# Kernel optimization log

Measured on AMD Instinct MI355X. Metric: run time of the kernel, lower is better.

## Reference

```python
import jax, jax.numpy as jnp
import numpy as np

N = 100000
E = 1600000
F_IN = 128
HID = 128
C = 10
NEG_SLOPE = 0.2


def setup_inputs() -> dict:
    key = jax.random.key(0)
    ks = jax.random.split(key, 12)
    x = jax.random.normal(ks[0], (N, F_IN), dtype=jnp.float32)
    edge_index = jax.random.randint(ks[1], (2, E), 0, N, dtype=jnp.int64)
    batch = jnp.zeros((N,), dtype=jnp.int64)
    s1 = 1.0 / np.sqrt(F_IN)
    s2 = 1.0 / np.sqrt(HID)
    return {
        "x": x,
        "edge_index": edge_index,
        "batch": batch,
        "W1": jax.random.normal(ks[2], (F_IN, HID), dtype=jnp.float32) * s1,
        "a_src1": jax.random.normal(ks[3], (HID,), dtype=jnp.float32) * s2,
        "a_dst1": jax.random.normal(ks[4], (HID,), dtype=jnp.float32) * s2,
        "b1": jnp.zeros((HID,), dtype=jnp.float32),
        "W2": jax.random.normal(ks[5], (HID, HID), dtype=jnp.float32) * s2,
        "a_src2": jax.random.normal(ks[6], (HID,), dtype=jnp.float32) * s2,
        "a_dst2": jax.random.normal(ks[7], (HID,), dtype=jnp.float32) * s2,
        "b2": jnp.zeros((HID,), dtype=jnp.float32),
        "Wlin": jax.random.normal(ks[8], (HID, C), dtype=jnp.float32) * s2,
        "blin": jnp.zeros((C,), dtype=jnp.float32),
    }


def gat_conv(x, src, dst, W, a_src, a_dst, b):
    # PyG GATConv, heads=1: h = xW; alpha_e = softmax_dst(leaky_relu(a_src.h[src] + a_dst.h[dst]))
    h = x @ W                                  # [N, H]
    alpha_s = h @ a_src                        # [N]
    alpha_d = h @ a_dst                        # [N]
    e = jax.nn.leaky_relu(alpha_s[src] + alpha_d[dst], NEG_SLOPE)  # [E]
    m = jax.ops.segment_max(e, dst, num_segments=N)                # per-dst max (stable softmax)
    ex = jnp.exp(e - m[dst])
    denom = jax.ops.segment_sum(ex, dst, num_segments=N)
    alpha = ex / (denom[dst] + 1e-16)          # [E]
    out = jax.ops.segment_sum(h[src] * alpha[:, None], dst, num_segments=N)
    return out + b


def reference(x, edge_index, batch, W1, a_src1, a_dst1, b1, W2, a_src2, a_dst2, b2, Wlin, blin):
    x = x.astype(jnp.float32)
    loops = jnp.arange(N, dtype=edge_index.dtype)
    src = jnp.concatenate([edge_index[0], loops])  # add_self_loops=True
    dst = jnp.concatenate([edge_index[1], loops])
    h = jax.nn.relu(gat_conv(x, src, dst, W1, a_src1, a_dst1, b1))
    h = jax.nn.relu(gat_conv(h, src, dst, W2, a_src2, a_dst2, b2))
    # dropout(p=0.5) is identity in eval mode
    return h @ Wlin + blin
```

## Files before the change

### kernel.cpp

```cpp
#include <hip/hip_runtime.h>

#define N_NODES 100000
#define N_EDGES 1600000
#define TOTE    (N_EDGES + N_NODES)
#define NEG     0.2f
#define NB      ((N_NODES + 255) >> 8)
#define BCAP    5120

typedef __attribute__((ext_vector_type(8))) short bf16x8;
typedef __attribute__((ext_vector_type(4))) float floatx4;

__device__ __forceinline__ unsigned short f2bf(float f) {
  unsigned int u = __float_as_uint(f);
  u += 0x7fffu + ((u >> 16) & 1u);
  return (unsigned short)(u >> 16);
}
__device__ __forceinline__ float bf_lo(unsigned int r) { return __uint_as_float(r << 16); }
__device__ __forceinline__ float bf_hi(unsigned int r) { return __uint_as_float(r & 0xffff0000u); }

__global__ __launch_bounds__(256) void k_wprep(const float* __restrict__ W1, const float* __restrict__ W2,
                                               unsigned short* __restrict__ B1hi, unsigned short* __restrict__ B1lo,
                                               unsigned short* __restrict__ B2hi, unsigned short* __restrict__ B2lo,
                                               int* __restrict__ bucketCnt) {
  int b = blockIdx.x;
  int t = threadIdx.x;
  if (b == 16) {
    for (int i = t; i < NB * 16; i += 256) bucketCnt[i] = 0;
    return;
  }
  const float* W = (b < 8) ? W1 : W2;
  unsigned short* Bh = (b < 8) ? B1hi : B2hi;
  unsigned short* Bl = (b < 8) ? B1lo : B2lo;
  int ntile = b & 7;
  int kq = t >> 6, lane = t & 63;
  int q = lane >> 4, m = lane & 15;
  int n = ntile * 16 + m;
  union { unsigned short us[8]; uint4 u4; } hi, lo;
#pragma unroll
  for (int j = 0; j < 8; ++j) {
    int k = kq * 32 + q * 8 + j;
    float w = W[(size_t)k * 128 + n];
    unsigned int u = __float_as_uint(w);
    hi.us[j] = (unsigned short)(u >> 16);
    float res = w - __uint_as_float(u & 0xffff0000u);
    lo.us[j] = f2bf(res);
  }
  size_t fo = ((size_t)(ntile * 4 + kq) * 64 + lane) * 8;
  *reinterpret_cast<uint4*>(Bh + fo) = hi.u4;
  *reinterpret_cast<uint4*>(Bl + fo) = lo.u4;
}

__global__ __launch_bounds__(256) void k_binA(const int* __restrict__ ei, int* __restrict__ bucketCnt,
                                              unsigned int* __restrict__ binned) {
  __shared__ int hist[NB];
  __shared__ int cur[NB];
  int t = threadIdx.x;
  for (int b = t; b < NB; b += 256) hist[b] = 0;
  __syncthreads();
  unsigned int pk[16]; int bk[16];
#pragma unroll
  for (int j = 0; j < 16; ++j) {
    int idx = blockIdx.x * 4096 + j * 256 + t;
    if (idx < N_EDGES) {
      int s = ei[idx], d = ei[N_EDGES + idx];
      bk[j] = d >> 8;
      pk[j] = ((unsigned int)s << 8) | (unsigned int)(d & 255);
      atomicAdd(&hist[bk[j]], 1);
    } else bk[j] = -1;
  }
  __syncthreads();
  for (int b = t; b < NB; b += 256) {
    int h = hist[b];
    if (h) cur[b] = b * BCAP + atomicAdd(&bucketCnt[b * 16], h);
  }
  __syncthreads();
#pragma unroll
  for (int j = 0; j < 16; ++j) {
    if (bk[j] >= 0) {
      int pos = atomicAdd(&cur[bk[j]], 1);
      binned[pos] = pk[j];
    }
  }
}

__global__ __launch_bounds__(512) void k_bin_scan(const int* __restrict__ bucketCnt,
                                                  int* __restrict__ binOffs) {
  __shared__ int sc[512];
  int t = threadIdx.x;
  int v = (t < NB) ? bucketCnt[t * 16] : 0;
  sc[t] = v; __syncthreads();
  for (int off = 1; off < 512; off <<= 1) {
    int x = (t >= off) ? sc[t - off] : 0;
    __syncthreads();
    sc[t] += x;
    __syncthreads();
  }
  int excl = sc[t] - v;
  if (t <= NB) binOffs[t] = excl;
}

__global__ __launch_bounds__(256) void k_binB(const unsigned int* __restrict__ binned,
                                              const int* __restrict__ binOffs,
                                              int* __restrict__ offs, int* __restrict__ srcs) {
  __shared__ int cnt[256];
  __shared__ int sc[256];
  __shared__ int cur[256];
  int b = blockIdx.x;
  int t = threadIdx.x;
  int node0 = b << 8;
  int nNodes = min(256, N_NODES - node0);
  int cntE = binOffs[b + 1] - binOffs[b];
  int e0 = b * BCAP, e1 = e0 + cntE;
  int base = binOffs[b] + node0;

  cnt[t] = 0; __syncthreads();
  for (int i = e0 + t; i < e1; i += 256) atomicAdd(&cnt[binned[i] & 255u], 1);
  __syncthreads();

  int v = (t < nNodes) ? cnt[t] + 1 : 0;
  sc[t] = v; __syncthreads();
  for (int off = 1; off < 256; off <<= 1) {
    int x = (t >= off) ? sc[t - off] : 0;
    __syncthreads();
    sc[t] += x;
    __syncthreads();
  }
  int excl = sc[t] - v;
  if (t < nNodes) {
    offs[node0 + t] = base + excl;
    srcs[base + excl] = node0 + t;
  }
  cur[t] = excl + 1;
  __syncthreads();

  for (int i = e0 + t; i < e1; i += 256) {
    unsigned int e = binned[i];
    int j = (int)(e & 255u);
    int s = (int)(e >> 8);
    int p = atomicAdd(&cur[j], 1);
    srcs[base + p] = s;
  }
  if (b == 0 && t == 0) offs[N_NODES] = TOTE;
}

template <bool SPLIT>
__global__ __launch_bounds__(256, 4) void k_gemm_mfma(const void* __restrict__ Aptr,
                                                   const unsigned short* __restrict__ Bhi,
                                                   const unsigned short* __restrict__ Blo,
                                                   unsigned short* __restrict__ Cb,
                                                   const float* __restrict__ avS, const float* __restrict__ avD,
                                                   float* __restrict__ aS, float* __restrict__ aD,
                                                   float* __restrict__ slotS, float* __restrict__ slotD) {
  constexpr int SRCB  = SPLIT ? 512 : 256;
  constexpr int ROWB  = SPLIT ? 528 : 272;
  constexpr int ABYTES = 64 * ROWB;
  constexpr int CHUNKS = ABYTES / 1024;
  __shared__ char sbuf[ABYTES];
  __shared__ float redS[64 * 4], redD[64 * 4];
  __shared__ float mS[64], mD[64];
  int t = threadIdx.x;
  int w = t >> 6, lane = t & 63;
  int q = lane >> 4, m = lane & 15;
  int rbase = blockIdx.x * 64;
  const char* Ab = (const char*)Aptr;

  for (int c = w; c < CHUNKS; c += 4) {
    int L = c * 1024 + lane * 16;
    int r = L / ROWB;
    int off = L - r * ROWB;
    int gr = min(rbase + r, N_NODES - 1);
    const char* src = (off < SRCB) ? (Ab + (size_t)gr * SRCB + off) : Ab;
    __builtin_amdgcn_global_load_lds((const __attribute__((address_space(1))) void*)src,
                                     (__attribute__((address_space(3))) void*)(sbuf + c * 1024),
                                     16, 0, 0);
  }

  floatx4 acc[4][2];
#pragma unroll
  for (int mt = 0; mt < 4; ++mt)
#pragma unroll
    for (int nt = 0; nt < 2; ++nt) acc[mt][nt] = (floatx4){0.f, 0.f, 0.f, 0.f};

  __syncthreads();

#pragma unroll
  for (int k0 = 0; k0 < 4; ++k0) {
    bf16x8 Bh[2], Bl[2], Ah[4], Al[4];
#pragma unroll
    for (int nt = 0; nt < 2; ++nt) {
      int ntg = w * 2 + nt;
      size_t fo = ((size_t)(ntg * 4 + k0) * 64 + lane) * 8;
      Bh[nt] = *reinterpret_cast<const bf16x8*>(Bhi + fo);
      Bl[nt] = *reinterpret_cast<const bf16x8*>(Blo + fo);
    }
#pragma unroll
    for (int mt = 0; mt < 4; ++mt) {
      int R = mt * 16 + m;
      if constexpr (SPLIT) {
        const char* ap = sbuf + R * ROWB + k0 * 128 + q * 32;
        float4 v0 = *reinterpret_cast<const float4*>(ap);
        float4 v1 = *reinterpret_cast<const float4*>(ap + 16);
        float av[8] = {v0.x, v0.y, v0.z, v0.w, v1.x, v1.y, v1.z, v1.w};
        union { unsigned short us[8]; bf16x8 v; } uh, ul;
#pragma unroll
        for (int j = 0; j < 8; ++j) {
          unsigned int u = __float_as_uint(av[j]);
          uh.us[j] = (unsigned short)(u >> 16);
          float res = av[j] - __uint_as_float(u & 0xffff0000u);
          ul.us[j] = f2bf(res);
        }
        Ah[mt] = uh.v; Al[mt] = ul.v;
      } else {
        Ah[mt] = *reinterpret_cast<const bf16x8*>(sbuf + R * ROWB + k0 * 64 + q * 16);
      }
    }
#pragma unroll
    for (int mt = 0; mt < 4; ++mt)
#pragma unroll
      for (int nt = 0; nt < 2; ++nt) {
        acc[mt][nt] = __builtin_amdgcn_mfma_f32_16x16x32_bf16(Ah[mt], Bh[nt], acc[mt][nt], 0, 0, 0);
        acc[mt][nt] = __builtin_amdgcn_mfma_f32_16x16x32_bf16(Ah[mt], Bl[nt], acc[mt][nt], 0, 0, 0);
        if constexpr (SPLIT)
          acc[mt][nt] = __builtin_amdgcn_mfma_f32_16x16x32_bf16(Al[mt], Bh[nt], acc[mt][nt], 0, 0, 0);
      }
  }

  float avs[2], avd[2];
#pragma unroll
  for (int nt = 0; nt < 2; ++nt) {
    int c = w * 32 + nt * 16 + m;
    avs[nt] = avS[c];
    avd[nt] = avD[c];
  }
#pragma unroll
  for (int mt = 0; mt < 4; ++mt)
#pragma unroll
    for (int r = 0; r < 4; ++r) {
      float ps = acc[mt][0][r] * avs[0] + acc[mt][1][r] * avs[1];
      float pd = acc[mt][0][r] * avd[0] + acc[mt][1][r] * avd[1];
      ps += __shfl_xor(ps, 1); pd += __shfl_xor(pd, 1);
      ps += __shfl_xor(ps, 2); pd += __shfl_xor(pd, 2);
      ps += __shfl_xor(ps, 4); pd += __shfl_xor(pd, 4);
      ps += __shfl_xor(ps, 8); pd += __shfl_xor(pd, 8);
      if (m == 0) {
        int rl = mt * 16 + q * 4 + r;
        redS[rl * 4 + w] = ps;
        redD[rl * 4 + w] = pd;
      }
    }

  __syncthreads();
  unsigned short* sC = (unsigned short*)sbuf;

#pragma unroll
  for (int mt = 0; mt < 4; ++mt)
#pragma unroll
    for (int nt = 0; nt < 2; ++nt)
#pragma unroll
      for (int r = 0; r < 4; ++r) {
        int rl = mt * 16 + q * 4 + r;
        int cl = w * 32 + nt * 16 + m;
        sC[rl * 136 + cl] = f2bf(acc[mt][nt][r]);
      }
  __syncthreads();

#pragma unroll
  for (int i = 0; i < 4; ++i) {
    int idx = i * 256 + t;
    int rl = idx >> 4, kk = idx & 15;
    int gr = rbase + rl;
    if (gr < N_NODES)
      *reinterpret_cast<uint4*>(Cb + (size_t)gr * 128 + kk * 8) =
          *reinterpret_cast<const uint4*>(sC + rl * 136 + kk * 8);
  }

  if (t < 64) {
    int gr = rbase + t;
    bool ok = gr < N_NODES;
    float ps = redS[t * 4] + redS[t * 4 + 1] + redS[t * 4 + 2] + redS[t * 4 + 3];
    float pd = redD[t * 4] + redD[t * 4 + 1] + redD[t * 4 + 2] + redD[t * 4 + 3];
    if (ok) { aS[gr] = ps; aD[gr] = pd; }
    mS[t] = ok ? ps : -1e30f;
    mD[t] = ok ? pd : -1e30f;
  }
  __syncthreads();
#pragma unroll
  for (int off = 32; off > 0; off >>= 1) {
    if (t < off) { mS[t] = fmaxf(mS[t], mS[t + off]); mD[t] = fmaxf(mD[t], mD[t + off]); }
    __syncthreads();
  }
  if (t == 0) { slotS[blockIdx.x] = mS[0]; slotD[blockIdx.x] = mD[0]; }
}

__global__ __launch_bounds__(256) void k_gmax(const float* __restrict__ slotS,
                                              const float* __restrict__ slotD,
                                              int n, float* __restrict__ gMh) {
  __shared__ float sS[256], sD[256];
  int t = threadIdx.x;
  float ms = -1e30f, md = -1e30f;
  for (int i = t; i < n; i += 256) { ms = fmaxf(ms, slotS[i]); md = fmaxf(md, slotD[i]); }
  sS[t] = ms; sD[t] = md;
  __syncthreads();
#pragma unroll
  for (int off = 128; off > 0; off >>= 1) {
    if (t < off) { sS[t] = fmaxf(sS[t], sS[t + off]); sD[t] = fmaxf(sD[t], sD[t + off]); }
    __syncthreads();
  }
  if (t == 0) {
    float M = sS[0] + sD[0];
    gMh[0] = (M > 0.f) ? M : NEG * M;
  }
}

#define FMA8(E, R)                                     \
  do {                                                 \
    acc[0] += (E) * bf_lo((R).x); acc[1] += (E) * bf_hi((R).x); \
    acc[2] += (E) * bf_lo((R).y); acc[3] += (E) * bf_hi((R).y); \
    acc[4] += (E) * bf_lo((R).z); acc[5] += (E) * bf_hi((R).z); \
    acc[6] += (E) * bf_lo((R).w); acc[7] += (E) * bf_hi((R).w); \
  } while (0)

#define LDG(R0, R1, R2, R3, E0, E1, E2, E3, J)                                                   \
  do {                                                                                           \
    float2 q0 = pairs[pbase + (J) + 0];                                                          \
    float2 q1 = pairs[pbase + (J) + 1];                                                          \
    float2 q2 = pairs[pbase + (J) + 2];                                                          \
    float2 q3 = pairs[pbase + (J) + 3];                                                          \
    E0 = q0.x; E1 = q1.x; E2 = q2.x; E3 = q3.x;                                                  \
    R0 = *reinterpret_cast<const uint4*>(hbl + ((size_t)(unsigned)__float_as_int(q0.y) << 7));   \
    R1 = *reinterpret_cast<const uint4*>(hbl + ((size_t)(unsigned)__float_as_int(q1.y) << 7));   \
    R2 = *reinterpret_cast<const uint4*>(hbl + ((size_t)(unsigned)__float_as_int(q2.y) << 7));   \
    R3 = *reinterpret_cast<const uint4*>(hbl + ((size_t)(unsigned)__float_as_int(q3.y) << 7));   \
  } while (0)
#define FMAG(R0, R1, R2, R3, E0, E1, E2, E3) \
  do { FMA8(E0, R0); FMA8(E1, R1); FMA8(E2, R2); FMA8(E3, R3); } while (0)

template <bool FINAL>
__global__ __launch_bounds__(256) void k_aggregate(const unsigned short* __restrict__ hb,
                                                   const float* __restrict__ aS,
                                                   const float* __restrict__ aD,
                                                   const int* __restrict__ offs,
                                                   const int* __restrict__ srcs,
                                                   const float* __restrict__ bias,
                                                   const float* __restrict__ gMh,
                                                   unsigned short* __restrict__ outb,
                                                   const float* __restrict__ Wl,
                                                   const float* __restrict__ bl,
                                                   float* __restrict__ out) {
  __shared__ float2 pairs[16 * 17];
  __shared__ float sWt[FINAL ? 10 * 144 : 1];
  __shared__ float sbl[FINAL ? 16 : 1];
  int t = threadIdx.x;
  if constexpr (FINAL) {
    if (t < 128) {
      int jj = t >> 5, ii = t & 31;
#pragma unroll
      for (int c = 0; c < 10; ++c) sWt[c * 144 + jj * 36 + ii] = Wl[t * 10 + c];
    }
    if (t < 10) sbl[t] = bl[t];
    __syncthreads();
  }
  int g = t >> 4;
  int l = t & 15;
  int dst = blockIdx.x * 16 + g;
  float Mh = gMh[0];
  int beg = offs[dst], end = offs[dst + 1];
  float adn = aD[dst];
  float denom = 0.f;
  float acc[8];
#pragma unroll
  for (int k = 0; k < 8; ++k) acc[k] = 0.f;
  const int pbase = g * 17;
  const unsigned short* hbl = hb + l * 8;

  uint4 ra0, ra1, ra2, ra3, rb0, rb1, rb2, rb3;
  float ea0, ea1, ea2, ea3, eb0, eb1, eb2, eb3;

  for (int chunk = beg; chunk < end; chunk += 16) {
    int i = chunk + l;
    float ex = 0.f; int s = 0;
    if (i < end) {
      s = srcs[i];
      float e = aS[s] + adn;
      e = (e > 0.f) ? e : NEG * e;
      ex = __expf(e - Mh);
    }
    denom += ex;
    pairs[pbase + l] = make_float2(ex, __int_as_float(s));
    int cnt = end - chunk; if (cnt > 16) cnt = 16;
    LDG(ra0, ra1, ra2, ra3, ea0, ea1, ea2, ea3, 0);
    int j = 0;
    for (;;) {
      bool more = (j + 4) < cnt;
      if (more) LDG(rb0, rb1, rb2, rb3, eb0, eb1, eb2, eb3, j + 4);
      FMAG(ra0, ra1, ra2, ra3, ea0, ea1, ea2, ea3);
      j += 4;
      if (!more) break;
      bool more2 = (j + 4) < cnt;
      if (more2) LDG(ra0, ra1, ra2, ra3, ea0, ea1, ea2, ea3, j + 4);
      FMAG(rb0, rb1, rb2, rb3, eb0, eb1, eb2, eb3);
      j += 4;
      if (!more2) break;
    }
  }

  denom += __shfl_xor(denom, 1);
  denom += __shfl_xor(denom, 2);
  denom += __shfl_xor(denom, 4);
  denom += __shfl_xor(denom, 8);
  float inv = 1.f / (denom + 1e-16f);
  float4 b0 = *reinterpret_cast<const float4*>(bias + l * 8);
  float4 b1 = *reinterpret_cast<const float4*>(bias + l * 8 + 4);
  float o0 = fmaxf(acc[0] * inv + b0.x, 0.f), o1 = fmaxf(acc[1] * inv + b0.y, 0.f);
  float o2 = fmaxf(acc[2] * inv + b0.z, 0.f), o3 = fmaxf(acc[3] * inv + b0.w, 0.f);
  float o4 = fmaxf(acc[4] * inv + b1.x, 0.f), o5 = fmaxf(acc[5] * inv + b1.y, 0.f);
  float o6 = fmaxf(acc[6] * inv + b1.z, 0.f), o7 = fmaxf(acc[7] * inv + b1.w, 0.f);

  if constexpr (!FINAL) {
    union { unsigned short us[8]; uint4 u4; } oo;
    oo.us[0] = f2bf(o0); oo.us[1] = f2bf(o1); oo.us[2] = f2bf(o2); oo.us[3] = f2bf(o3);
    oo.us[4] = f2bf(o4); oo.us[5] = f2bf(o5); oo.us[6] = f2bf(o6); oo.us[7] = f2bf(o7);
    *reinterpret_cast<uint4*>(outb + (size_t)dst * 128 + l * 8) = oo.u4;
  } else {
    float p[10];
#pragma unroll
    for (int c = 0; c < 10; ++c) {
      const float4* wp = reinterpret_cast<const float4*>(&sWt[c * 144 + (l >> 2) * 36 + (l & 3) * 8]);
      float4 w0 = wp[0], w1 = wp[1];
      p[c] = o0 * w0.x + o1 * w0.y + o2 * w0.z + o3 * w0.w +
             o4 * w1.x + o5 * w1.y + o6 * w1.z + o7 * w1.w;
    }
#pragma unroll
    for (int c = 0; c < 10; ++c) {
      p[c] += __shfl_xor(p[c], 1);
      p[c] += __shfl_xor(p[c], 2);
      p[c] += __shfl_xor(p[c], 4);
      p[c] += __shfl_xor(p[c], 8);
    }
    if (l == 0) {
      float* orow = out + (size_t)dst * 10;
      *reinterpret_cast<float2*>(orow + 0) = make_float2(p[0] + sbl[0], p[1] + sbl[1]);
      *reinterpret_cast<float2*>(orow + 2) = make_float2(p[2] + sbl[2], p[3] + sbl[3]);
      *reinterpret_cast<float2*>(orow + 4) = make_float2(p[4] + sbl[4], p[5] + sbl[5]);
      *reinterpret_cast<float2*>(orow + 6) = make_float2(p[6] + sbl[6], p[7] + sbl[7]);
      *reinterpret_cast<float2*>(orow + 8) = make_float2(p[8] + sbl[8], p[9] + sbl[9]);
    }
  }
}

extern "C" void kernel_launch(void* const* d_in, const int* in_sizes, int n_in,
                              void* d_out, int out_size, void* d_ws, size_t ws_size,
                              hipStream_t stream) {
  const float* x   = (const float*)d_in[0];
  const int*   ei  = (const int*)d_in[1];
  const float* W1  = (const float*)d_in[3];
  const float* as1 = (const float*)d_in[4];
  const float* ad1 = (const float*)d_in[5];
  const float* b1  = (const float*)d_in[6];
  const float* W2  = (const float*)d_in[7];
  const float* as2 = (const float*)d_in[8];
  const float* ad2 = (const float*)d_in[9];
  const float* b2  = (const float*)d_in[10];
  const float* Wl  = (const float*)d_in[11];
  const float* bl  = (const float*)d_in[12];
  float* out = (float*)d_out;

  char* p = (char*)d_ws;
  unsigned short* hb   = (unsigned short*)p; p += (size_t)N_NODES * 128 * sizeof(unsigned short);
  unsigned short* hagg = (unsigned short*)p; p += (size_t)N_NODES * 128 * sizeof(unsigned short);
  float* aS    = (float*)p; p += (size_t)N_NODES * sizeof(float);
  float* aD    = (float*)p; p += (size_t)N_NODES * sizeof(float);
  int* offs    = (int*)p;   p += (size_t)(N_NODES + 4) * sizeof(int);
  int* srcs    = (int*)p;   p += (size_t)TOTE * sizeof(int);
  int* bucketCnt = (int*)p; p += (size_t)NB * 16 * sizeof(int);
  int* binOffs   = (int*)p; p += (size_t)(NB + 4) * sizeof(int);
  float* slotS = (float*)p; p += 2048 * sizeof(float);
  float* slotD = (float*)p; p += 2048 * sizeof(float);
  float* gMh = (float*)p;   p += 4 * sizeof(float);
  unsigned short* B1hi = (unsigned short*)p; p += 128 * 128 * sizeof(unsigned short);
  unsigned short* B1lo = (unsigned short*)p; p += 128 * 128 * sizeof(unsigned short);
  unsigned short* B2hi = (unsigned short*)p; p += 128 * 128 * sizeof(unsigned short);
  unsigned short* B2lo = (unsigned short*)p; p += 128 * 128 * sizeof(unsigned short);
  unsigned int* binned = (unsigned int*)hagg;

  int binBlocks = (N_EDGES + 4095) / 4096;

  k_wprep<<<17, 256, 0, stream>>>(W1, W2, B1hi, B1lo, B2hi, B2lo, bucketCnt);
  k_binA<<<binBlocks, 256, 0, stream>>>(ei, bucketCnt, binned);
  k_bin_scan<<<1, 512, 0, stream>>>(bucketCnt, binOffs);
  k_binB<<<NB, 256, 0, stream>>>(binned, binOffs, offs, srcs);

  int gemmBlocks = (N_NODES + 63) / 64;
  int aggBlocks  = N_NODES / 16;

  k_gemm_mfma<true><<<gemmBlocks, 256, 0, stream>>>(x, B1hi, B1lo, hb, as1, ad1, aS, aD, slotS, slotD);
  k_gmax<<<1, 256, 0, stream>>>(slotS, slotD, gemmBlocks, gMh);
  k_aggregate<false><<<aggBlocks, 256, 0, stream>>>(hb, aS, aD, offs, srcs, b1, gMh, hagg,
                                                    nullptr, nullptr, nullptr);
  k_gemm_mfma<false><<<gemmBlocks, 256, 0, stream>>>(hagg, B2hi, B2lo, hb, as2, ad2, aS, aD, slotS, slotD);
  k_gmax<<<1, 256, 0, stream>>>(slotS, slotD, gemmBlocks, gMh);
  k_aggregate<true><<<aggBlocks, 256, 0, stream>>>(hb, aS, aD, offs, srcs, b2, gMh, hagg,
                                                   Wl, bl, out);
}
```

Baseline: 333.3 us.

## Fuse edge binning pass and first-layer GEMM into one heterogeneous launch

Merges the edge-binning kernel and the layer-1 MFMA GEMM into a single launch whose first 391 blocks bin edges and whose remaining blocks compute xW1 plus attention projections. The two workloads are independent, so running them side by side lets memory-bound binning overlap with the GEMM and drops one launch. The shared-memory union sizes every block for the GEMM's LDS footprint, which may lower occupancy for the binning blocks, and the GEMM is specialised to fp32 input.

After: 325.1 us (median of 2 runs). 1.03x faster.

```diff
diff --git a/kernel.cpp b/kernel.cpp
--- a/kernel.cpp
+++ b/kernel.cpp
@@ -6,6 +6,7 @@
 #define NEG     0.2f
 #define NB      ((N_NODES + 255) >> 8)
 #define BCAP    5120
+#define BINBLK  391
 
 typedef __attribute__((ext_vector_type(8))) short bf16x8;
 typedef __attribute__((ext_vector_type(4))) float floatx4;
@@ -50,37 +51,181 @@
   *reinterpret_cast<uint4*>(Bl + fo) = lo.u4;
 }
 
-__global__ __launch_bounds__(256) void k_binA(const int* __restrict__ ei, int* __restrict__ bucketCnt,
-                                              unsigned int* __restrict__ binned) {
-  __shared__ int hist[NB];
-  __shared__ int cur[NB];
+__global__ __launch_bounds__(256, 4) void k_binA_gemm1(
+    const int* __restrict__ ei, int* __restrict__ bucketCnt, unsigned int* __restrict__ binned,
+    const float* __restrict__ x,
+    const unsigned short* __restrict__ Bhi, const unsigned short* __restrict__ Blo,
+    unsigned short* __restrict__ Cb,
+    const float* __restrict__ avS, const float* __restrict__ avD,
+    float* __restrict__ aS, float* __restrict__ aD,
+    float* __restrict__ slotS, float* __restrict__ slotD) {
+  __shared__ union {
+    struct { int hist[NB]; int cur[NB]; } a;
+    struct { char sbuf[64 * 528]; float redS[256]; float redD[256];
+             float mS[64]; float mD[64]; } g;
+  } sm;
   int t = threadIdx.x;
-  for (int b = t; b < NB; b += 256) hist[b] = 0;
-  __syncthreads();
-  unsigned int pk[16]; int bk[16];
-#pragma unroll
-  for (int j = 0; j < 16; ++j) {
-    int idx = blockIdx.x * 4096 + j * 256 + t;
-    if (idx < N_EDGES) {
-      int s = ei[idx], d = ei[N_EDGES + idx];
-      bk[j] = d >> 8;
-      pk[j] = ((unsigned int)s << 8) | (unsigned int)(d & 255);
-      atomicAdd(&hist[bk[j]], 1);
-    } else bk[j] = -1;
-  }
-  __syncthreads();
-  for (int b = t; b < NB; b += 256) {
-    int h = hist[b];
-    if (h) cur[b] = b * BCAP + atomicAdd(&bucketCnt[b * 16], h);
-  }
-  __syncthreads();
-#pragma unroll
-  for (int j = 0; j < 16; ++j) {
-    if (bk[j] >= 0) {
-      int pos = atomicAdd(&cur[bk[j]], 1);
-      binned[pos] = pk[j];
-    }
-  }
+
+  if (blockIdx.x < BINBLK) {
+    for (int b = t; b < NB; b += 256) sm.a.hist[b] = 0;
+    __syncthreads();
+    unsigned int pk[16]; int bk[16];
+#pragma unroll
+    for (int j = 0; j < 16; ++j) {
+      int idx = blockIdx.x * 4096 + j * 256 + t;
+      if (idx < N_EDGES) {
+        int s = ei[idx], d = ei[N_EDGES + idx];
+        bk[j] = d >> 8;
+        pk[j] = ((unsigned int)s << 8) | (unsigned int)(d & 255);
+        atomicAdd(&sm.a.hist[bk[j]], 1);
+      } else bk[j] = -1;
+    }
+    __syncthreads();
+    for (int b = t; b < NB; b += 256) {
+      int h = sm.a.hist[b];
+      if (h) sm.a.cur[b] = b * BCAP + atomicAdd(&bucketCnt[b * 16], h);
+    }
+    __syncthreads();
+#pragma unroll
+    for (int j = 0; j < 16; ++j) {
+      if (bk[j] >= 0) {
+        int pos = atomicAdd(&sm.a.cur[bk[j]], 1);
+        binned[pos] = pk[j];
+      }
+    }
+    return;
+  }
+
+  int bid = blockIdx.x - BINBLK;
+  int w = t >> 6, lane = t & 63;
+  int q = lane >> 4, m = lane & 15;
+  int rbase = bid * 64;
+  const char* Ab = (const char*)x;
+
+  for (int c = w; c < 33; c += 4) {
+    int L = c * 1024 + lane * 16;
+    int r = L / 528;
+    int off = L - r * 528;
+    int gr = min(rbase + r, N_NODES - 1);
+    const char* src = (off < 512) ? (Ab + (size_t)gr * 512 + off) : Ab;
+    __builtin_amdgcn_global_load_lds((const __attribute__((address_space(1))) void*)src,
+                                     (__attribute__((address_space(3))) void*)(sm.g.sbuf + c * 1024),
+                                     16, 0, 0);
+  }
+
+  floatx4 acc[4][2];
+#pragma unroll
+  for (int mt = 0; mt < 4; ++mt)
+#pragma unroll
+    for (int nt = 0; nt < 2; ++nt) acc[mt][nt] = (floatx4){0.f, 0.f, 0.f, 0.f};
+
+  __syncthreads();
+
+#pragma unroll
+  for (int k0 = 0; k0 < 4; ++k0) {
+    bf16x8 Bh[2], Bl[2], Ah[4], Al[4];
+#pragma unroll
+    for (int nt = 0; nt < 2; ++nt) {
+      int ntg = w * 2 + nt;
+      size_t fo = ((size_t)(ntg * 4 + k0) * 64 + lane) * 8;
+      Bh[nt] = *reinterpret_cast<const bf16x8*>(Bhi + fo);
+      Bl[nt] = *reinterpret_cast<const bf16x8*>(Blo + fo);
+    }
+#pragma unroll
+    for (int mt = 0; mt < 4; ++mt) {
+      int R = mt * 16 + m;
+      const char* ap = sm.g.sbuf + R * 528 + k0 * 128 + q * 32;
+      float4 v0 = *reinterpret_cast<const float4*>(ap);
+      float4 v1 = *reinterpret_cast<const float4*>(ap + 16);
+      float av[8] = {v0.x, v0.y, v0.z, v0.w, v1.x, v1.y, v1.z, v1.w};
+      union { unsigned short us[8]; bf16x8 v; } uh, ul;
+#pragma unroll
+      for (int j = 0; j < 8; ++j) {
+        unsigned int u = __float_as_uint(av[j]);
+        uh.us[j] = (unsigned short)(u >> 16);
+        float res = av[j] - __uint_as_float(u & 0xffff0000u);
+        ul.us[j] = f2bf(res);
+      }
+      Ah[mt] = uh.v; Al[mt] = ul.v;
+    }
+#pragma unroll
+    for (int mt = 0; mt < 4; ++mt)
+#pragma unroll
+      for (int nt = 0; nt < 2; ++nt) {
+        acc[mt][nt] = __builtin_amdgcn_mfma_f32_16x16x32_bf16(Ah[mt], Bh[nt], acc[mt][nt], 0, 0, 0);
+        acc[mt][nt] = __builtin_amdgcn_mfma_f32_16x16x32_bf16(Ah[mt], Bl[nt], acc[mt][nt], 0, 0, 0);
+        acc[mt][nt] = __builtin_amdgcn_mfma_f32_16x16x32_bf16(Al[mt], Bh[nt], acc[mt][nt], 0, 0, 0);
+      }
+  }
+
+  float avs[2], avd[2];
+#pragma unroll
+  for (int nt = 0; nt < 2; ++nt) {
+    int c = w * 32 + nt * 16 + m;
+    avs[nt] = avS[c];
+    avd[nt] = avD[c];
+  }
+#pragma unroll
+  for (int mt = 0; mt < 4; ++mt)
+#pragma unroll
+    for (int r = 0; r < 4; ++r) {
+      float ps = acc[mt][0][r] * avs[0] + acc[mt][1][r] * avs[1];
+      float pd = acc[mt][0][r] * avd[0] + acc[mt][1][r] * avd[1];
+      ps += __shfl_xor(ps, 1); pd += __shfl_xor(pd, 1);
+      ps += __shfl_xor(ps, 2); pd += __shfl_xor(pd, 2);
+      ps += __shfl_xor(ps, 4); pd += __shfl_xor(pd, 4);
+      ps += __shfl_xor(ps, 8); pd += __shfl_xor(pd, 8);
+      if (m == 0) {
+        int rl = mt * 16 + q * 4 + r;
+        sm.g.redS[rl * 4 + w] = ps;
+        sm.g.redD[rl * 4 + w] = pd;
+      }
+    }
+
+  __syncthreads();
+  unsigned short* sC = (unsigned short*)sm.g.sbuf;
+
+#pragma unroll
+  for (int mt = 0; mt < 4; ++mt)
+#pragma unroll
+    for (int nt = 0; nt < 2; ++nt)
+#pragma unroll
+      for (int r = 0; r < 4; ++r) {
+        int rl = mt * 16 + q * 4 + r;
+        int cl = w * 32 + nt * 16 + m;
+        sC[rl * 136 + cl] = f2bf(acc[mt][nt][r]);
+      }
+  __syncthreads();
+
+#pragma unroll
+  for (int i = 0; i < 4; ++i) {
+    int idx = i * 256 + t;
+    int rl = idx >> 4, kk = idx & 15;
+    int gr = rbase + rl;
+    if (gr < N_NODES)
+      *reinterpret_cast<uint4*>(Cb + (size_t)gr * 128 + kk * 8) =
+          *reinterpret_cast<const uint4*>(sC + rl * 136 + kk * 8);
+  }
+
+  if (t < 64) {
+    int gr = rbase + t;
+    bool ok = gr < N_NODES;
+    float ps = sm.g.redS[t * 4] + sm.g.redS[t * 4 + 1] + sm.g.redS[t * 4 + 2] + sm.g.redS[t * 4 + 3];
+    float pd = sm.g.redD[t * 4] + sm.g.redD[t * 4 + 1] + sm.g.redD[t * 4 + 2] + sm.g.redD[t * 4 + 3];
+    if (ok) { aS[gr] = ps; aD[gr] = pd; }
+    sm.g.mS[t] = ok ? ps : -1e30f;
+    sm.g.mD[t] = ok ? pd : -1e30f;
+  }
+  __syncthreads();
+#pragma unroll
+  for (int off = 32; off > 0; off >>= 1) {
+    if (t < off) {
+      sm.g.mS[t] = fmaxf(sm.g.mS[t], sm.g.mS[t + off]);
+      sm.g.mD[t] = fmaxf(sm.g.mD[t], sm.g.mD[t + off]);
+    }
+    __syncthreads();
+  }
+  if (t == 0) { slotS[bid] = sm.g.mS[0]; slotD[bid] = sm.g.mD[0]; }
 }
 
 __global__ __launch_bounds__(512) void k_bin_scan(const int* __restrict__ bucketCnt,
@@ -483,17 +628,15 @@
   unsigned short* B2lo = (unsigned short*)p; p += 128 * 128 * sizeof(unsigned short);
   unsigned int* binned = (unsigned int*)hagg;
 
-  int binBlocks = (N_EDGES + 4095) / 4096;
+  int gemmBlocks = (N_NODES + 63) / 64;
+  int aggBlocks  = N_NODES / 16;
 
   k_wprep<<<17, 256, 0, stream>>>(W1, W2, B1hi, B1lo, B2hi, B2lo, bucketCnt);
-  k_binA<<<binBlocks, 256, 0, stream>>>(ei, bucketCnt, binned);
+  k_binA_gemm1<<<BINBLK + gemmBlocks, 256, 0, stream>>>(ei, bucketCnt, binned,
+                                                        x, B1hi, B1lo, hb, as1, ad1,
+                                                        aS, aD, slotS, slotD);
   k_bin_scan<<<1, 512, 0, stream>>>(bucketCnt, binOffs);
   k_binB<<<NB, 256, 0, stream>>>(binned, binOffs, offs, srcs);
-
-  int gemmBlocks = (N_NODES + 63) / 64;
-  int aggBlocks  = N_NODES / 16;
-
-  k_gemm_mfma<true><<<gemmBlocks, 256, 0, stream>>>(x, B1hi, B1lo, hb, as1, ad1, aS, aD, slotS, slotD);
   k_gmax<<<1, 256, 0, stream>>>(slotS, slotD, gemmBlocks, gMh);
   k_aggregate<false><<<aggBlocks, 256, 0, stream>>>(hb, aS, aD, offs, srcs, b1, gMh, hagg,
                                                     nullptr, nullptr, nullptr);
```
